# Kernel tuning notes

Measured on AMD Instinct MI355X. Metric: run time of the kernel, lower is better.

Reference implementation:

```python
import jax, jax.numpy as jnp
import numpy as np

L = 6       # n_layers
D = 1024    # d_model
H = 16      # n_heads
HD = D // H
DF = 4096   # d_ff
E = 8       # n_experts
K = 2       # top_k
V = 32000   # vocab
B = 2
S = 1024    # seq_len == max_seq_len


def setup_inputs() -> dict:
    key = jax.random.key(0)
    ks = iter(jax.random.split(key, 40))
    n = lambda shape: jax.random.normal(next(ks), shape, dtype=jnp.float32) * 0.02
    return {
        'input_ids': jax.random.randint(next(ks), (B, S), 0, V),
        'tok_emb': n((V, D)),
        'pos_emb': n((S, D)),
        'attn_in_w': n((L, 3 * D, D)),   # packed q,k,v in_proj (torch MultiheadAttention)
        'attn_in_b': jnp.zeros((L, 3 * D), jnp.float32),
        'attn_out_w': n((L, D, D)),
        'attn_out_b': jnp.zeros((L, D), jnp.float32),
        'ln1_w': jnp.ones((L, D), jnp.float32),
        'ln1_b': jnp.zeros((L, D), jnp.float32),
        'ln2_w': jnp.ones((L, D), jnp.float32),
        'ln2_b': jnp.zeros((L, D), jnp.float32),
        'ffn_w1': n((L, DF, D)),
        'ffn_b1': jnp.zeros((L, DF), jnp.float32),
        'ffn_w2': n((L, D, DF)),
        'ffn_b2': jnp.zeros((L, D), jnp.float32),
        'gate_w': n((L // 2, E, D)),     # router gate for the 3 MoE (odd) layers
        'lnf_w': jnp.ones((D,), jnp.float32),
        'lnf_b': jnp.zeros((D,), jnp.float32),
        'head_w': n((V, D)),
    }


def _ln(x, w, b):
    m = x.mean(-1, keepdims=True)
    v = x.var(-1, keepdims=True)
    return (x - m) / jnp.sqrt(v + 1e-5) * w + b


def _mha(x, in_w, in_b, out_w, out_b):
    b_, s_, _ = x.shape
    qkv = x @ in_w.T + in_b
    q, k, v = jnp.split(qkv, 3, axis=-1)
    rs = lambda t: t.reshape(b_, s_, H, HD)
    q, k, v = rs(q), rs(k), rs(v)
    scores = jnp.einsum('bqhd,bkhd->bhqk', q, k) / np.sqrt(HD).astype(np.float32)
    causal = jnp.tril(jnp.ones((s_, s_), bool))
    scores = jnp.where(causal[None, None], scores, -jnp.inf)
    a = jax.nn.softmax(scores, axis=-1)
    o = jnp.einsum('bhqk,bkhd->bqhd', a, v).reshape(b_, s_, D)
    return o @ out_w.T + out_b


def reference(input_ids, tok_emb, pos_emb, attn_in_w, attn_in_b, attn_out_w,
              attn_out_b, ln1_w, ln1_b, ln2_w, ln2_b, ffn_w1, ffn_b1, ffn_w2,
              ffn_b2, gate_w, lnf_w, lnf_b, head_w):
    s = input_ids.shape[1]
    x = tok_emb[input_ids] + pos_emb[jnp.arange(s)][None]  # [B,S,D]
    aux = jnp.float32(0.0)
    for i in range(L):
        h = _ln(x + _mha(x, attn_in_w[i], attn_in_b[i], attn_out_w[i], attn_out_b[i]),
                ln1_w[i], ln1_b[i])
        ffn = jax.nn.relu(h @ ffn_w1[i].T + ffn_b1[i]) @ ffn_w2[i].T + ffn_b2[i]
        if i % 2 == 1:  # MoE layer; source shares ONE expert module across all experts
            gi = i // 2
            probs = jax.nn.softmax(h @ gate_w[gi].T, axis=-1)     # [B,S,E]
            topv, topi = jax.lax.top_k(probs, K)
            ffn = ffn * topv.sum(-1, keepdims=True)               # combine top-k weights
            me = probs.mean((0, 1))                               # mean gate prob per expert
            ce = jax.nn.one_hot(topi[..., 0], E, dtype=probs.dtype).mean((0, 1))
            aux = aux + E * jnp.sum(me * ce)                      # load-balancing aux loss
        x = _ln(h + ffn, ln2_w[i], ln2_b[i])
    x = _ln(x, lnf_w, lnf_b)
    logits = x @ head_w.T  # [B,S,V]
    return (logits, aux)
```

## Files before the change

kernel.cpp:

```cpp
#include <hip/hip_runtime.h>
#include <hip/hip_bf16.h>

typedef __hip_bfloat16 bf16;
typedef __bf16 bf16x8 __attribute__((ext_vector_type(8)));
typedef float f32x4 __attribute__((ext_vector_type(4)));
typedef short s16x8 __attribute__((ext_vector_type(8)));
typedef unsigned short u16;

#define NL 6
#define DM 1024
#define NH 16
#define HD 64
#define DF 4096
#define NE 8
#define NV 32000
#define NB 2
#define NS 1024
#define NT (NB*NS)

__device__ __forceinline__ float ldin(const void* p, long i, int isf32) {
    return isf32 ? ((const float*)p)[i]
                 : __bfloat162float(((const bf16*)p)[i]);
}

__global__ __launch_bounds__(256)
void cvt_k(const void* __restrict__ src, bf16* __restrict__ dst, long n,
           const u16* __restrict__ probe)
{
    int isf32 = (probe[0] != (u16)0x3F80);
    long stride = (long)gridDim.x * 256 * 8;
    for (long i = ((long)blockIdx.x * 256 + threadIdx.x) * 8; i < n; i += stride) {
        if (isf32) {
            const float* s = (const float*)src + i;
            f32x4 f0 = *(const f32x4*)s;
            f32x4 f1 = *(const f32x4*)(s + 4);
            s16x8 o;
            #pragma unroll
            for (int jj = 0; jj < 4; ++jj) {
                bf16 v0 = __float2bfloat16(f0[jj]);
                bf16 v1 = __float2bfloat16(f1[jj]);
                o[jj]   = *(short*)&v0;
                o[4+jj] = *(short*)&v1;
            }
            *(s16x8*)&dst[i] = o;
        } else {
            *(s16x8*)&dst[i] = *(const s16x8*)((const u16*)src + i);
        }
    }
}

template<int TMI, int WF32, int WB16, int RELU>
__global__ __launch_bounds__(256)
void gemm128(const u16* __restrict__ A, const u16* __restrict__ B,
             const void* __restrict__ bias, long biasoff,
             const u16* __restrict__ probe,
             float* __restrict__ Cf, bf16* __restrict__ Cb,
             int M, int N, int K, int lda, int ldb, int ldc, float alpha)
{
    int isf32 = (probe[0] != (u16)0x3F80);
    int bm = blockIdx.x, bn = blockIdx.y;

    __shared__ __align__(16) u16 As[TMI*32*64];
    __shared__ __align__(16) u16 Bs[128*64];

    int t = threadIdx.x;
    int lane = t & 63, wv = t >> 6;
    int wr = wv >> 1, wc = wv & 1;
    int rsel = lane & 15, grp = lane >> 4;

    f32x4 acc[TMI][4] = {};

    const u16* Ag = A + (long)(bm * (TMI*32)) * lda;
    const u16* Bg = B + (long)(bn * 128) * ldb;
    int sub = lane >> 3;
    int csw = ((lane & 7) ^ sub) * 8;

    for (int kt = 0; kt < K; kt += 64) {
        __syncthreads();
        #pragma unroll
        for (int i = 0; i < TMI; ++i) {
            int row = wv*(TMI*8) + i*8;
            __builtin_amdgcn_global_load_lds(
                (const __attribute__((address_space(1))) void*)(Ag + (long)(row + sub)*lda + kt + csw),
                (__attribute__((address_space(3))) void*)(As + row*64),
                16, 0, 0);
        }
        #pragma unroll
        for (int i = 0; i < 4; ++i) {
            int row = wv*32 + i*8;
            __builtin_amdgcn_global_load_lds(
                (const __attribute__((address_space(1))) void*)(Bg + (long)(row + sub)*ldb + kt + csw),
                (__attribute__((address_space(3))) void*)(Bs + row*64),
                16, 0, 0);
        }
        __syncthreads();
        #pragma unroll
        for (int kk = 0; kk < 2; ++kk) {
            int js = ((kk*4 + grp) ^ (rsel & 7)) * 8;
            bf16x8 af[TMI], bf[4];
            #pragma unroll
            for (int mi = 0; mi < TMI; ++mi)
                af[mi] = *(const bf16x8*)&As[(wr*(TMI*16) + mi*16 + rsel)*64 + js];
            #pragma unroll
            for (int ni = 0; ni < 4; ++ni)
                bf[ni] = *(const bf16x8*)&Bs[(wc*64 + ni*16 + rsel)*64 + js];
            #pragma unroll
            for (int mi = 0; mi < TMI; ++mi)
                #pragma unroll
                for (int ni = 0; ni < 4; ++ni)
                    acc[mi][ni] = __builtin_amdgcn_mfma_f32_16x16x32_bf16(
                        af[mi], bf[ni], acc[mi][ni], 0, 0, 0);
        }
    }

    #pragma unroll
    for (int mi = 0; mi < TMI; ++mi)
    #pragma unroll
    for (int ni = 0; ni < 4; ++ni)
    #pragma unroll
    for (int j = 0; j < 4; ++j) {
        int row = bm*(TMI*32) + wr*(TMI*16) + mi*16 + grp*4 + j;
        int col = bn*128 + wc*64 + ni*16 + rsel;
        float v = acc[mi][ni][j] * alpha;
        if (bias) v += ldin(bias, biasoff + col, isf32);
        if (RELU) v = fmaxf(v, 0.f);
        long ci = (long)row * ldc + col;
        if (WF32) Cf[ci] = v;
        if (WB16) Cb[ci] = __float2bfloat16(v);
    }
}

__global__ __launch_bounds__(256)
void gemm64f(const u16* __restrict__ A, const void* __restrict__ B,
             const u16* __restrict__ probe, float* __restrict__ Cf,
             int M, int N, int K, int lda, int ldb, int ldc)
{
    int isf32 = (probe[0] != (u16)0x3F80);
    int bn = blockIdx.x, bm = blockIdx.y;
    __shared__ __align__(16) u16 As[64*72];
    __shared__ __align__(16) u16 Bs[64*72];
    int t = threadIdx.x;
    int lane = t & 63, wv = t >> 6;
    int wm = (wv >> 1) * 32, wn = (wv & 1) * 32;
    int rsel = lane & 15, grp = lane >> 4;
    f32x4 acc[2][2] = {};
    const u16* Ag = A + (long)(bm * 64) * lda;
    int r0 = t >> 3, c8 = (t & 7) * 8;
    for (int kt = 0; kt < K; kt += 64) {
        __syncthreads();
        #pragma unroll
        for (int p = 0; p < 2; ++p) {
            int r = r0 + 32 * p;
            *(s16x8*)&As[r*72 + c8] = *(const s16x8*)(Ag + (long)r * lda + kt + c8);
        }
        if (isf32) {
            const float* Bg = (const float*)B + (long)(bn * 64) * ldb;
            #pragma unroll
            for (int p = 0; p < 2; ++p) {
                int r = r0 + 32 * p;
                const float* src = Bg + (long)r * ldb + kt + c8;
                f32x4 f0 = *(const f32x4*)src;
                f32x4 f1 = *(const f32x4*)(src + 4);
                s16x8 o8;
                #pragma unroll
                for (int jj = 0; jj < 4; ++jj) {
                    bf16 v0 = __float2bfloat16(f0[jj]);
                    bf16 v1 = __float2bfloat16(f1[jj]);
                    o8[jj]   = *(short*)&v0;
                    o8[4+jj] = *(short*)&v1;
                }
                *(s16x8*)&Bs[r*72 + c8] = o8;
            }
        } else {
            const u16* Bg = (const u16*)B + (long)(bn * 64) * ldb;
            #pragma unroll
            for (int p = 0; p < 2; ++p) {
                int r = r0 + 32 * p;
                *(s16x8*)&Bs[r*72 + c8] = *(const s16x8*)(Bg + (long)r * ldb + kt + c8);
            }
        }
        __syncthreads();
        #pragma unroll
        for (int kk = 0; kk < 64; kk += 32) {
            bf16x8 a0 = *(const bf16x8*)&As[(wm +      rsel)*72 + kk + grp*8];
            bf16x8 a1 = *(const bf16x8*)&As[(wm + 16 + rsel)*72 + kk + grp*8];
            bf16x8 b0 = *(const bf16x8*)&Bs[(wn +      rsel)*72 + kk + grp*8];
            bf16x8 b1 = *(const bf16x8*)&Bs[(wn + 16 + rsel)*72 + kk + grp*8];
            acc[0][0] = __builtin_amdgcn_mfma_f32_16x16x32_bf16(a0, b0, acc[0][0], 0, 0, 0);
            acc[0][1] = __builtin_amdgcn_mfma_f32_16x16x32_bf16(a0, b1, acc[0][1], 0, 0, 0);
            acc[1][0] = __builtin_amdgcn_mfma_f32_16x16x32_bf16(a1, b0, acc[1][0], 0, 0, 0);
            acc[1][1] = __builtin_amdgcn_mfma_f32_16x16x32_bf16(a1, b1, acc[1][1], 0, 0, 0);
        }
    }
    #pragma unroll
    for (int mi = 0; mi < 2; ++mi)
    #pragma unroll
    for (int ni = 0; ni < 2; ++ni)
    #pragma unroll
    for (int j = 0; j < 4; ++j) {
        int row = bm*64 + wm + 16*mi + grp*4 + j;
        int col = bn*64 + wn + 16*ni + rsel;
        Cf[(long)row * ldc + col] = acc[mi][ni][j];
    }
}

__global__ __launch_bounds__(256)
void flash_k(const u16* __restrict__ qkv, bf16* __restrict__ o)
{
    int qt = blockIdx.x;
    int z  = blockIdx.y;
    int b = z >> 4, h = z & 15;

    __shared__ __align__(16) u16 Qs[64*72];
    __shared__ __align__(16) u16 Ks[64*72];
    __shared__ __align__(16) u16 Vt[64*72];
    __shared__ __align__(16) u16 Ps[4*16*72];

    int t = threadIdx.x;
    int lane = t & 63, wv = t >> 6;
    int rsel = lane & 15, grp = lane >> 4;

    const u16* base = qkv + (long)(b*NS) * (3*DM) + h*HD;

    {
        const u16* qb = base + (long)(qt*64) * (3*DM);
        #pragma unroll
        for (int u = 0; u < 2; ++u) {
            int id = t + u*256;
            int r = id >> 3, c = (id & 7) * 8;
            *(s16x8*)&Qs[r*72 + c] = *(const s16x8*)(qb + (long)r*(3*DM) + c);
        }
    }
    __syncthreads();
    bf16x8 qf[2];
    #pragma unroll
    for (int kk = 0; kk < 2; ++kk)
        qf[kk] = *(const bf16x8*)&Qs[(wv*16 + rsel)*72 + kk*32 + grp*8];

    float m[4], l[4];
    f32x4 acc_o[4] = {};
    #pragma unroll
    for (int j = 0; j < 4; ++j) { m[j] = -3.0e38f; l[j] = 0.f; }

    for (int kt = 0; kt <= qt; ++kt) {
        __syncthreads();
        const u16* kb = base + (long)(kt*64) * (3*DM) + DM;
        const u16* vb = base + (long)(kt*64) * (3*DM) + 2*DM;
        #pragma unroll
        for (int u = 0; u < 2; ++u) {
            int id = t + u*256;
            int r = id >> 3, c = (id & 7) * 8;
            *(s16x8*)&Ks[r*72 + c] = *(const s16x8*)(kb + (long)r*(3*DM) + c);
            s16x8 vv = *(const s16x8*)(vb + (long)r*(3*DM) + c);
            #pragma unroll
            for (int jj = 0; jj < 8; ++jj)
                Vt[(c+jj)*72 + r] = ((u16*)&vv)[jj];
        }
        __syncthreads();

        f32x4 s[4] = {};
        #pragma unroll
        for (int kk = 0; kk < 2; ++kk) {
            #pragma unroll
            for (int ni = 0; ni < 4; ++ni) {
                bf16x8 bf = *(const bf16x8*)&Ks[(16*ni + rsel)*72 + kk*32 + grp*8];
                s[ni] = __builtin_amdgcn_mfma_f32_16x16x32_bf16(qf[kk], bf, s[ni], 0, 0, 0);
            }
        }
        float sv[4][4];
        int rloc = wv*16 + grp*4;
        #pragma unroll
        for (int ni = 0; ni < 4; ++ni)
        #pragma unroll
        for (int j = 0; j < 4; ++j) {
            float x = s[ni][j] * 0.125f;
            if (kt == qt && (16*ni + rsel) > (rloc + j)) x = -3.0e38f;
            sv[ni][j] = x;
        }
        float pm[4];
        #pragma unroll
        for (int j = 0; j < 4; ++j)
            pm[j] = fmaxf(fmaxf(sv[0][j], sv[1][j]), fmaxf(sv[2][j], sv[3][j]));
        #pragma unroll
        for (int msk = 1; msk < 16; msk <<= 1)
            #pragma unroll
            for (int j = 0; j < 4; ++j)
                pm[j] = fmaxf(pm[j], __shfl_xor(pm[j], msk));

        float mn[4], sc[4], ps[4];
        #pragma unroll
        for (int j = 0; j < 4; ++j) {
            mn[j] = fmaxf(m[j], pm[j]);
            sc[j] = __expf(m[j] - mn[j]);
            ps[j] = 0.f;
        }
        u16* pw = &Ps[wv*16*72];
        #pragma unroll
        for (int ni = 0; ni < 4; ++ni)
        #pragma unroll
        for (int j = 0; j < 4; ++j) {
            float p = __expf(sv[ni][j] - mn[j]);
            ps[j] += p;
            bf16 pb = __float2bfloat16(p);
            pw[(grp*4 + j)*72 + 16*ni + rsel] = *(u16*)&pb;
        }
        #pragma unroll
        for (int msk = 1; msk < 16; msk <<= 1)
            #pragma unroll
            for (int j = 0; j < 4; ++j)
                ps[j] += __shfl_xor(ps[j], msk);
        #pragma unroll
        for (int j = 0; j < 4; ++j) {
            l[j] = l[j]*sc[j] + ps[j];
            m[j] = mn[j];
        }
        #pragma unroll
        for (int ni = 0; ni < 4; ++ni)
        #pragma unroll
        for (int j = 0; j < 4; ++j)
            acc_o[ni][j] *= sc[j];

        __syncthreads();

        #pragma unroll
        for (int kk = 0; kk < 2; ++kk) {
            bf16x8 pa = *(const bf16x8*)&pw[rsel*72 + kk*32 + grp*8];
            #pragma unroll
            for (int ni = 0; ni < 4; ++ni) {
                bf16x8 vf = *(const bf16x8*)&Vt[(16*ni + rsel)*72 + kk*32 + grp*8];
                acc_o[ni] = __builtin_amdgcn_mfma_f32_16x16x32_bf16(pa, vf, acc_o[ni], 0, 0, 0);
            }
        }
    }

    #pragma unroll
    for (int j = 0; j < 4; ++j) {
        int q = qt*64 + wv*16 + grp*4 + j;
        float inv = 1.f / l[j];
        #pragma unroll
        for (int ni = 0; ni < 4; ++ni) {
            int d = 16*ni + rsel;
            o[(long)(b*NS + q)*DM + h*HD + d] = __float2bfloat16(acc_o[ni][j] * inv);
        }
    }
}

__global__ __launch_bounds__(256)
void embed_k(const int* __restrict__ ids, const void* __restrict__ te,
             const void* __restrict__ pe, const u16* __restrict__ probe,
             float* __restrict__ xf, bf16* __restrict__ xb)
{
    int isf32 = (probe[0] != (u16)0x3F80);
    int tk = blockIdx.x;
    int s = tk & (NS-1);
    long idb = (long)ids[tk] * DM;
    #pragma unroll
    for (int u = 0; u < 4; ++u) {
        int d = threadIdx.x + u*256;
        float v = ldin(te, idb + d, isf32) + ldin(pe, (long)s*DM + d, isf32);
        xf[(long)tk*DM + d] = v;
        xb[(long)tk*DM + d] = __float2bfloat16(v);
    }
}

__global__ __launch_bounds__(256)
void ln_k(const float* __restrict__ in1, const float* __restrict__ in2,
          const float* __restrict__ rsc, const void* __restrict__ w, long woff,
          const void* __restrict__ b, long boff, const u16* __restrict__ probe,
          float* __restrict__ of, bf16* __restrict__ ob)
{
    int isf32 = (probe[0] != (u16)0x3F80);
    int row = blockIdx.x;
    int t = threadIdx.x;
    const float* p1 = in1 + (long)row * DM;
    float sc = rsc ? rsc[row] : 1.f;
    float v[4], s = 0.f;
    #pragma unroll
    for (int u = 0; u < 4; ++u) {
        int d = t + u*256;
        float x = p1[d];
        if (in2) x += sc * in2[(long)row*DM + d];
        v[u] = x; s += x;
    }
    __shared__ float r1[4], r2[4];
    int lane = t & 63, wv = t >> 6;
    #pragma unroll
    for (int msk = 32; msk; msk >>= 1) s += __shfl_xor(s, msk);
    if (lane == 0) r1[wv] = s;
    __syncthreads();
    float mean = (r1[0]+r1[1]+r1[2]+r1[3]) * (1.f/DM);
    float vs = 0.f;
    #pragma unroll
    for (int u = 0; u < 4; ++u) { float d0 = v[u] - mean; vs += d0*d0; }
    #pragma unroll
    for (int msk = 32; msk; msk >>= 1) vs += __shfl_xor(vs, msk);
    if (lane == 0) r2[wv] = vs;
    __syncthreads();
    float var = (r2[0]+r2[1]+r2[2]+r2[3]) * (1.f/DM);
    float rstd = rsqrtf(var + 1e-5f);
    #pragma unroll
    for (int u = 0; u < 4; ++u) {
        int d = t + u*256;
        float y = (v[u] - mean) * rstd * ldin(w, woff + d, isf32) + ldin(b, boff + d, isf32);
        if (of) of[(long)row*DM + d] = y;
        if (ob) ob[(long)row*DM + d] = __float2bfloat16(y);
    }
}

__global__ __launch_bounds__(256)
void router_k(const float* __restrict__ h, const void* __restrict__ gwp, long goff,
              const u16* __restrict__ probe,
              float* __restrict__ scale, float* __restrict__ mece)
{
    int isf32 = (probe[0] != (u16)0x3F80);
    int lane = threadIdx.x & 63, wv = threadIdx.x >> 6;
    int base = blockIdx.x * 64 + wv * 16;

    float me_loc[NE], ce_loc[NE];
    #pragma unroll
    for (int e = 0; e < NE; ++e) { me_loc[e] = 0.f; ce_loc[e] = 0.f; }

    for (int j = 0; j < 16; ++j) {
        int tk = base + j;
        const float* hr = h + (long)tk * DM;
        float part[NE];
        #pragma unroll
        for (int e = 0; e < NE; ++e) part[e] = 0.f;
        #pragma unroll 4
        for (int i = 0; i < 16; ++i) {
            int d = lane + 64*i;
            float hv = hr[d];
            #pragma unroll
            for (int e = 0; e < NE; ++e)
                part[e] += hv * ldin(gwp, goff + e*DM + d, isf32);
        }
        #pragma unroll
        for (int e = 0; e < NE; ++e)
            #pragma unroll
            for (int msk = 32; msk; msk >>= 1)
                part[e] += __shfl_xor(part[e], msk);
        float mx = part[0];
        #pragma unroll
        for (int e = 1; e < NE; ++e) mx = fmaxf(mx, part[e]);
        float ex[NE], sum = 0.f;
        #pragma unroll
        for (int e = 0; e < NE; ++e) { ex[e] = __expf(part[e] - mx); sum += ex[e]; }
        float inv = 1.f / sum;
        int i1 = 0; float v1 = ex[0]*inv;
        #pragma unroll
        for (int e = 1; e < NE; ++e) { float p = ex[e]*inv; if (p > v1) { v1 = p; i1 = e; } }
        float v2 = -1.f;
        #pragma unroll
        for (int e = 0; e < NE; ++e) { float p = ex[e]*inv; if (e != i1 && p > v2) v2 = p; }
        if (lane == 0) {
            scale[tk] = v1 + v2;
            #pragma unroll
            for (int e = 0; e < NE; ++e) me_loc[e] += ex[e]*inv;
            ce_loc[i1] += 1.f;
        }
    }

    __shared__ float red[4][2*NE];
    if (lane == 0) {
        #pragma unroll
        for (int e = 0; e < NE; ++e) {
            red[wv][e]      = me_loc[e];
            red[wv][NE + e] = ce_loc[e];
        }
    }
    __syncthreads();
    if (threadIdx.x < 2*NE) {
        float s = red[0][threadIdx.x] + red[1][threadIdx.x]
                + red[2][threadIdx.x] + red[3][threadIdx.x];
        atomicAdd(&mece[threadIdx.x], s);
    }
}

__global__ void auxfin_k(const float* __restrict__ me, const float* __restrict__ ce,
                         float* __restrict__ aux)
{
    float s = 0.f;
    for (int e = 0; e < NE; ++e) s += me[e] * ce[e];
    *aux += (float)NE * s * (1.f / ((float)NT * (float)NT));
}

__global__ void zerof(float* p, int n)
{
    int i = blockIdx.x * 64 + threadIdx.x;
    if (i < n) p[i] = 0.f;
}

__global__ void write_aux_f32_k(float* dst, const float* aux)
{
    *dst = *aux;
}

extern "C" void kernel_launch(void* const* d_in, const int* in_sizes, int n_in,
                              void* d_out, int out_size, void* d_ws, size_t ws_size,
                              hipStream_t stream)
{
    const int*  ids     = (const int*)d_in[0];
    const void* tok_emb = d_in[1];
    const void* pos_emb = d_in[2];
    const void* ain_w   = d_in[3];
    const void* ain_b   = d_in[4];
    const void* aout_w  = d_in[5];
    const void* aout_b  = d_in[6];
    const u16*  probe   = (const u16*)d_in[7];
    const void* ln1w    = d_in[7];
    const void* ln1b    = d_in[8];
    const void* ln2w    = d_in[9];
    const void* ln2b    = d_in[10];
    const void* fw1     = d_in[11];
    const void* fb1     = d_in[12];
    const void* fw2     = d_in[13];
    const void* fb2     = d_in[14];
    const void* gw      = d_in[15];
    const void* lnfw    = d_in[16];
    const void* lnfb    = d_in[17];
    const void* headw   = d_in[18];
    float* out = (float*)d_out;

    char* op = (char*)d_out;
    auto oalloc = [&](size_t n) { char* p = op; op += (n + 255) & ~(size_t)255; return p; };
    bf16*  f1_b   = (bf16*) oalloc((size_t)NT*DF*2);
    bf16*  qkv_b  = (bf16*) oalloc((size_t)NT*3*DM*2);
    float* tmp_f  = (float*)oalloc((size_t)NT*DM*4);
    bf16*  o_b    = (bf16*) oalloc((size_t)NT*DM*2);
    bf16*  h_b    = (bf16*) oalloc((size_t)NT*DM*2);
    float* x_f    = (float*)oalloc((size_t)NT*DM*4);
    float* h_f    = (float*)oalloc((size_t)NT*DM*4);
    bf16*  wc_ain = (bf16*) oalloc((size_t)NL*3*DM*DM*2);
    bf16*  wc_aout= (bf16*) oalloc((size_t)NL*DM*DM*2);
    bf16*  wc_fw1 = (bf16*) oalloc((size_t)NL*DF*DM*2);
    bf16*  wc_fw2 = (bf16*) oalloc((size_t)NL*DM*DF*2);

    char* wp = (char*)d_ws;
    auto alloc = [&](size_t n) { char* p = wp; wp += (n + 255) & ~(size_t)255; return p; };
    bf16*  x_b    = (bf16*) alloc((size_t)NT*DM*2);
    float* scale  = (float*)alloc((size_t)NT*4);
    float* mece   = (float*)alloc(16*4);
    float* aux    = (float*)alloc(4);
    size_t ws_used = (size_t)(wp - (char*)d_ws);
    bool head_cvt = (ws_size >= ws_used + (size_t)NV*DM*2 + 256);
    bf16* wc_head = head_cvt ? (bf16*)alloc((size_t)NV*DM*2) : nullptr;

    auto cvt = [&](const void* src, bf16* dst, long n) {
        int blocks = (int)((n/8 + 255) / 256); if (blocks > 2048) blocks = 2048;
        cvt_k<<<blocks, 256, 0, stream>>>(src, dst, n, probe);
    };

    zerof<<<1, 64, 0, stream>>>(aux, 1);
    cvt(ain_w,  wc_ain,  (long)NL*3*DM*DM);
    cvt(aout_w, wc_aout, (long)NL*DM*DM);
    cvt(fw1,    wc_fw1,  (long)NL*DF*DM);
    cvt(fw2,    wc_fw2,  (long)NL*DM*DF);
    if (head_cvt) cvt(headw, wc_head, (long)NV*DM);

    embed_k<<<NT, 256, 0, stream>>>(ids, tok_emb, pos_emb, probe, x_f, x_b);

    for (int i = 0; i < NL; ++i) {
        gemm128<4,0,1,0><<<dim3(NT/128, 3*DM/128), 256, 0, stream>>>(
            (const u16*)x_b, (const u16*)(wc_ain + (size_t)i*3*DM*DM),
            ain_b, (long)i*3*DM, probe,
            nullptr, qkv_b, NT, 3*DM, DM, DM, DM, 3*DM, 1.f);
        flash_k<<<dim3(NS/64, NB*NH), 256, 0, stream>>>((const u16*)qkv_b, o_b);
        gemm128<2,1,0,0><<<dim3(NT/64, DM/128), 256, 0, stream>>>(
            (const u16*)o_b, (const u16*)(wc_aout + (size_t)i*DM*DM),
            aout_b, (long)i*DM, probe,
            tmp_f, nullptr, NT, DM, DM, DM, DM, DM, 1.f);
        ln_k<<<NT, 256, 0, stream>>>(x_f, tmp_f, nullptr, ln1w, (long)i*DM, ln1b, (long)i*DM,
                                     probe, h_f, h_b);
        gemm128<4,0,1,1><<<dim3(NT/128, DF/128), 256, 0, stream>>>(
            (const u16*)h_b, (const u16*)(wc_fw1 + (size_t)i*DF*DM),
            fb1, (long)i*DF, probe,
            nullptr, f1_b, NT, DF, DM, DM, DM, DF, 1.f);
        gemm128<2,1,0,0><<<dim3(NT/64, DM/128), 256, 0, stream>>>(
            (const u16*)f1_b, (const u16*)(wc_fw2 + (size_t)i*DM*DF),
            fb2, (long)i*DM, probe,
            tmp_f, nullptr, NT, DM, DF, DF, DF, DM, 1.f);
        const float* sc = nullptr;
        if (i & 1) {
            zerof<<<1, 64, 0, stream>>>(mece, 16);
            router_k<<<NT/64, 256, 0, stream>>>(h_f, gw, (long)(i/2)*NE*DM, probe,
                                                scale, mece);
            auxfin_k<<<1, 1, 0, stream>>>(mece, mece + 8, aux);
            sc = scale;
        }
        ln_k<<<NT, 256, 0, stream>>>(h_f, tmp_f, sc, ln2w, (long)i*DM, ln2b, (long)i*DM,
                                     probe, x_f, x_b);
    }
    ln_k<<<NT, 256, 0, stream>>>(x_f, nullptr, nullptr, lnfw, 0, lnfb, 0, probe, nullptr, x_b);
    if (head_cvt) {
        gemm128<4,1,0,0><<<dim3(NT/128, NV/128), 256, 0, stream>>>(
            (const u16*)x_b, (const u16*)wc_head, nullptr, 0, probe,
            out, nullptr, NT, NV, DM, DM, DM, NV, 1.f);
    } else {
        gemm64f<<<dim3(NV/64, NT/64), 256, 0, stream>>>(
            (const u16*)x_b, headw, probe, out, NT, NV, DM, DM, DM, NV);
    }
    write_aux_f32_k<<<1, 1, 0, stream>>>(out + (size_t)NT*NV, aux);
}
```

Measured before the change: 2.047 ms.

## Pre-transpose V and double-buffer K/V tiles via async global-to-LDS loads

Adds a separate kernel that writes V transposed per head to a scratch buffer, so flash attention no longer scatters V element by element into shared memory. The flash kernel now loads K and V tiles with asynchronous global_load_lds into double-buffered, XOR-swizzled shared memory and prefetches the next tile while computing the current one. This is meant to cut LDS transpose cost and hide global load latency. The cost is an extra launch and an extra round trip of V through global memory per layer.

```diff
diff --git a/kernel.cpp b/kernel.cpp
--- a/kernel.cpp
+++ b/kernel.cpp
@@ -205,33 +205,80 @@
 }
 
 __global__ __launch_bounds__(256)
-void flash_k(const u16* __restrict__ qkv, bf16* __restrict__ o)
+void vtrans_k(const u16* __restrict__ qkv, u16* __restrict__ vt)
+{
+    int st = blockIdx.x;
+    int z  = blockIdx.y;
+    int b = z >> 4, h = z & 15;
+    __shared__ u16 T[64*72];
+    int t = threadIdx.x;
+    int r = t >> 3, c8 = (t & 7) * 8;
+    const u16* src = qkv + (long)(b*NS + st*64) * (3*DM) + 2*DM + h*HD;
+    #pragma unroll
+    for (int p = 0; p < 2; ++p) {
+        int s = r + p*32;
+        *(s16x8*)&T[s*72 + c8] = *(const s16x8*)(src + (long)s*(3*DM) + c8);
+    }
+    __syncthreads();
+    u16* dst = vt + (long)z*HD*NS + (long)st*64;
+    #pragma unroll
+    for (int p = 0; p < 2; ++p) {
+        int d = r + p*32;
+        u16 tmp[8];
+        #pragma unroll
+        for (int j = 0; j < 8; ++j) tmp[j] = T[(c8+j)*72 + d];
+        *(s16x8*)(dst + (long)d*NS + c8) = *(s16x8*)tmp;
+    }
+}
+
+__global__ __launch_bounds__(256)
+void flash_k(const u16* __restrict__ qkv, const u16* __restrict__ vt,
+             bf16* __restrict__ o)
 {
     int qt = blockIdx.x;
     int z  = blockIdx.y;
     int b = z >> 4, h = z & 15;
 
     __shared__ __align__(16) u16 Qs[64*72];
-    __shared__ __align__(16) u16 Ks[64*72];
-    __shared__ __align__(16) u16 Vt[64*72];
+    __shared__ __align__(16) u16 Ks[2][64*64];
+    __shared__ __align__(16) u16 Vs[2][64*64];
     __shared__ __align__(16) u16 Ps[4*16*72];
 
     int t = threadIdx.x;
     int lane = t & 63, wv = t >> 6;
     int rsel = lane & 15, grp = lane >> 4;
-
-    const u16* base = qkv + (long)(b*NS) * (3*DM) + h*HD;
+    int sub = lane >> 3, csw = ((lane & 7) ^ sub) * 8;
+
+    const u16* qbase = qkv + (long)(b*NS) * (3*DM) + h*HD;
+    const u16* kbase = qbase + DM;
+    const u16* vbase = vt + (long)z*HD*NS;
 
     {
-        const u16* qb = base + (long)(qt*64) * (3*DM);
         #pragma unroll
         for (int u = 0; u < 2; ++u) {
             int id = t + u*256;
             int r = id >> 3, c = (id & 7) * 8;
-            *(s16x8*)&Qs[r*72 + c] = *(const s16x8*)(qb + (long)r*(3*DM) + c);
-        }
-    }
+            *(s16x8*)&Qs[r*72 + c] = *(const s16x8*)(qbase + (long)(qt*64 + r)*(3*DM) + c);
+        }
+    }
+
+    auto stage = [&](int buf, int kt) {
+        #pragma unroll
+        for (int i = 0; i < 2; ++i) {
+            int row = wv*16 + i*8;
+            __builtin_amdgcn_global_load_lds(
+                (const __attribute__((address_space(1))) void*)(kbase + (long)(kt*64 + row + sub)*(3*DM) + csw),
+                (__attribute__((address_space(3))) void*)(&Ks[buf][row*64]),
+                16, 0, 0);
+            __builtin_amdgcn_global_load_lds(
+                (const __attribute__((address_space(1))) void*)(vbase + (long)(row + sub)*NS + kt*64 + csw),
+                (__attribute__((address_space(3))) void*)(&Vs[buf][row*64]),
+                16, 0, 0);
+        }
+    };
+    stage(0, 0);
     __syncthreads();
+
     bf16x8 qf[2];
     #pragma unroll
     for (int kk = 0; kk < 2; ++kk)
@@ -243,27 +290,16 @@
     for (int j = 0; j < 4; ++j) { m[j] = -3.0e38f; l[j] = 0.f; }
 
     for (int kt = 0; kt <= qt; ++kt) {
-        __syncthreads();
-        const u16* kb = base + (long)(kt*64) * (3*DM) + DM;
-        const u16* vb = base + (long)(kt*64) * (3*DM) + 2*DM;
-        #pragma unroll
-        for (int u = 0; u < 2; ++u) {
-            int id = t + u*256;
-            int r = id >> 3, c = (id & 7) * 8;
-            *(s16x8*)&Ks[r*72 + c] = *(const s16x8*)(kb + (long)r*(3*DM) + c);
-            s16x8 vv = *(const s16x8*)(vb + (long)r*(3*DM) + c);
-            #pragma unroll
-            for (int jj = 0; jj < 8; ++jj)
-                Vt[(c+jj)*72 + r] = ((u16*)&vv)[jj];
-        }
-        __syncthreads();
+        int cur = kt & 1;
+        if (kt < qt) stage(cur ^ 1, kt + 1);
 
         f32x4 s[4] = {};
         #pragma unroll
         for (int kk = 0; kk < 2; ++kk) {
+            int js = ((kk*4 + grp) ^ (rsel & 7)) * 8;
             #pragma unroll
             for (int ni = 0; ni < 4; ++ni) {
-                bf16x8 bf = *(const bf16x8*)&Ks[(16*ni + rsel)*72 + kk*32 + grp*8];
+                bf16x8 bf = *(const bf16x8*)&Ks[cur][(16*ni + rsel)*64 + js];
                 s[ni] = __builtin_amdgcn_mfma_f32_16x16x32_bf16(qf[kk], bf, s[ni], 0, 0, 0);
             }
         }
@@ -324,13 +360,15 @@
 
         #pragma unroll
         for (int kk = 0; kk < 2; ++kk) {
+            int js = ((kk*4 + grp) ^ (rsel & 7)) * 8;
             bf16x8 pa = *(const bf16x8*)&pw[rsel*72 + kk*32 + grp*8];
             #pragma unroll
             for (int ni = 0; ni < 4; ++ni) {
-                bf16x8 vf = *(const bf16x8*)&Vt[(16*ni + rsel)*72 + kk*32 + grp*8];
+                bf16x8 vf = *(const bf16x8*)&Vs[cur][(16*ni + rsel)*64 + js];
                 acc_o[ni] = __builtin_amdgcn_mfma_f32_16x16x32_bf16(pa, vf, acc_o[ni], 0, 0, 0);
             }
         }
+        __syncthreads();
     }
 
     #pragma unroll
@@ -530,6 +568,7 @@
     bf16*  h_b    = (bf16*) oalloc((size_t)NT*DM*2);
     float* x_f    = (float*)oalloc((size_t)NT*DM*4);
     float* h_f    = (float*)oalloc((size_t)NT*DM*4);
+    u16*   vt     = (u16*)  oalloc((size_t)NB*NH*HD*NS*2);
     bf16*  wc_ain = (bf16*) oalloc((size_t)NL*3*DM*DM*2);
     bf16*  wc_aout= (bf16*) oalloc((size_t)NL*DM*DM*2);
     bf16*  wc_fw1 = (bf16*) oalloc((size_t)NL*DF*DM*2);
@@ -564,7 +603,8 @@
             (const u16*)x_b, (const u16*)(wc_ain + (size_t)i*3*DM*DM),
             ain_b, (long)i*3*DM, probe,
             nullptr, qkv_b, NT, 3*DM, DM, DM, DM, 3*DM, 1.f);
-        flash_k<<<dim3(NS/64, NB*NH), 256, 0, stream>>>((const u16*)qkv_b, o_b);
+        vtrans_k<<<dim3(NS/64, NB*NH), 256, 0, stream>>>((const u16*)qkv_b, vt);
+        flash_k<<<dim3(NS/64, NB*NH), 256, 0, stream>>>((const u16*)qkv_b, vt, o_b);
         gemm128<2,1,0,0><<<dim3(NT/64, DM/128), 256, 0, stream>>>(
             (const u16*)o_b, (const u16*)(wc_aout + (size_t)i*DM*DM),
             aout_b, (long)i*DM, probe,
```

After: 1.939 ms. -5.3%, faster.
